# Performance work log

Measured on AMD Instinct MI355X. Metric: run time of the kernel, lower is better.

The kernel has to match this reference:

```python
import jax, jax.numpy as jnp
import numpy as np

LAYERS = (256, 256, 256)
SPLIT = True


def setup_inputs() -> dict:
    key = jax.random.key(0)
    ks = jax.random.split(key, 4)
    B, F0, D = 512, 40, 32
    # field_num with split=True: [40, 128, 128, 128]
    fnum = [F0]
    for i, s in enumerate(LAYERS):
        fnum.append(s // 2 if (SPLIT and i < len(LAYERS) - 1) else (s // 2 if SPLIT else s))
    # conv input channels per layer: fnum[i] * F0
    c1, c2, c3 = fnum[0] * F0, fnum[1] * F0, fnum[2] * F0  # 1600, 5120, 5120
    inputs = jax.random.normal(ks[0], (B, F0, D), dtype=jnp.float32)
    W1 = jax.random.normal(ks[1], (c1, LAYERS[0]), dtype=jnp.float32) / jnp.sqrt(jnp.float32(c1))
    W2 = jax.random.normal(ks[2], (c2, LAYERS[1]), dtype=jnp.float32) / jnp.sqrt(jnp.float32(c2))
    W3 = jax.random.normal(ks[3], (c3, LAYERS[2]), dtype=jnp.float32) / jnp.sqrt(jnp.float32(c3))
    b1 = jnp.zeros((LAYERS[0],), dtype=jnp.float32)
    b2 = jnp.zeros((LAYERS[1],), dtype=jnp.float32)
    b3 = jnp.zeros((LAYERS[2],), dtype=jnp.float32)
    return {"inputs": inputs, "W1": W1, "b1": b1, "W2": W2, "b2": b2, "W3": W3, "b3": b3}


def _cin_forward(inputs, params):
    # inputs: [B, F0, D]
    B, F0, D = inputs.shape
    x0 = inputs
    h = inputs
    outputs = []
    n = len(params)
    for i, (W, b) in enumerate(params):
        # Per-embedding-dim outer product: [B, D, Fi, F0] -> flatten channels.
        z = jnp.einsum('bfd,bgd->bdfg', h, x0).reshape(B, D, -1)
        # 1x1 Conv1D over length-D axis == dense projection on channel axis.
        y = z @ W + b                     # [B, D, size]
        y = jax.nn.relu(y)
        y = jnp.transpose(y, (0, 2, 1))   # [B, size, D]
        if SPLIT and i < n - 1:
            half = y.shape[1] // 2
            outputs.append(y[:, :half, :])
            h = y[:, half:, :]
        else:
            outputs.append(y)
            h = y
    pooled = jnp.concatenate(outputs, axis=1)  # [B, sum_out_fields, D]
    return jnp.sum(pooled, axis=2)             # [B, sum_out_fields]


def reference(inputs, W1, b1, W2, b2, W3, b3):
    return _cin_forward(inputs, [(W1, b1), (W2, b2), (W3, b3)])
```

## Files before the change

### kernel.cpp

```cpp
#include <hip/hip_runtime.h>
#include <hip/hip_bf16.h>


typedef __attribute__((ext_vector_type(8))) short short8;
typedef __attribute__((ext_vector_type(4))) float f32x4;

#define DEVINL __device__ __forceinline__

DEVINL float bf16f(unsigned short u) {
  return __builtin_bit_cast(float, ((unsigned int)u) << 16);
}
DEVINL unsigned short f2bf(float f) {
  unsigned int u = __builtin_bit_cast(unsigned int, f);
  u = u + 0x7FFFu + ((u >> 16) & 1u);
  return (unsigned short)(u >> 16);
}
DEVINL unsigned int pk2(float lo, float hi) {
  union { __hip_bfloat162 h; unsigned int u; } cv;
  cv.h = __float22bfloat162_rn(make_float2(lo, hi));
  return cv.u;
}
DEVINL void gl_lds16(const unsigned short* g, unsigned short* l) {
  __builtin_amdgcn_global_load_lds(
      (const __attribute__((address_space(1))) unsigned int*)g,
      (__attribute__((address_space(3))) unsigned int*)l, 16, 0, 0);
}

__global__ void prep_x(const float* __restrict__ in, unsigned short* __restrict__ xT) {
  __shared__ float lf[40 * 33];
  const int b = blockIdx.x, t = threadIdx.x;
  for (int i = t; i < 1280; i += 256) {
    int g = i >> 5, d = i & 31;
    lf[g * 33 + d] = in[b * 1280 + i];
  }
  __syncthreads();
  for (int i = t; i < 1280; i += 256) {
    int d = i / 40, g = i % 40;
    xT[b * 1280 + i] = f2bf(lf[g * 33 + d]);
  }
}

__global__ void prep_w(const float* __restrict__ W1, const float* __restrict__ W2,
                       const float* __restrict__ W3, unsigned short* __restrict__ Wf1,
                       unsigned short* __restrict__ Wf2, unsigned short* __restrict__ Wf3) {
  __shared__ float lw[8192];
  const int bid = blockIdx.x, t = threadIdx.x;
  const float* W; unsigned short* dst; int s, SPW;
  if (bid < 50)       { W = W1; dst = Wf1; s = bid;       SPW = 10; }
  else if (bid < 210) { W = W2; dst = Wf2; s = bid - 50;  SPW = 32; }
  else                { W = W3; dst = Wf3; s = bid - 210; SPW = 32; }
  const int smod = s % SPW, w = s / SPW;
  for (int i = t; i < 8192; i += 256) {
    int kl = i >> 8, col = i & 255;
    int f = 4 * smod + (kl >> 3);
    int g = 8 * w + (kl & 7);
    lw[i] = W[(f * 40 + g) * 256 + col];
  }
  __syncthreads();
  for (int c = t; c < 1024; c += 256) {
    int grp = c >> 6, ll = c & 63;
    int qq = ll >> 4, col = grp * 16 + (ll & 15);
    unsigned short u[8];
#pragma unroll
    for (int j = 0; j < 8; ++j) u[j] = f2bf(lw[(qq * 8 + j) * 256 + col]);
    uint4 v;
    v.x = (unsigned)u[0] | ((unsigned)u[1] << 16);
    v.y = (unsigned)u[2] | ((unsigned)u[3] << 16);
    v.z = (unsigned)u[4] | ((unsigned)u[5] << 16);
    v.w = (unsigned)u[6] | ((unsigned)u[7] << 16);
    *(uint4*)&dst[s * 8192 + c * 8] = v;
  }
}

template <int LAYER>
__global__ __launch_bounds__(256, 2) void cin_layer(
    const unsigned short* __restrict__ Wfrag, const unsigned short* __restrict__ xT,
    const unsigned short* __restrict__ hIn, const float* __restrict__ bias,
    unsigned short* __restrict__ hOut, float* __restrict__ out) {
  constexpr int FIN = (LAYER == 1) ? 40 : 128;
  constexpr int NKT = FIN * 40 / 32;
  constexpr int SPW = FIN / 4;
  constexpr int HP = 144;

  constexpr int SM_SHORTS = (LAYER == 1) ? (4096 + 5120) : (4096 + 128 * HP);
  __shared__ __align__(16) unsigned short smem[SM_SHORTS];
  unsigned short* Bb = smem;
  unsigned short* hx = smem + 4096;

  const int tid = threadIdx.x;
  const int l = tid & 63;
  const int wid = tid >> 6;
  const int q = l >> 4;
  const int bm = blockIdx.x >> 2;
  const int tn = blockIdx.x & 3;
  const int r0 = bm * 128;
  const int b0 = bm * 4;

  gl_lds16(Wfrag + tn * 2048 + tid * 8, Bb + tid * 8);

  if constexpr (LAYER > 1) {
    const unsigned short* hsrc = hIn + bm * (128 * HP);
#pragma unroll
    for (int i = 0; i < 9; ++i)
      gl_lds16(hsrc + i * 2048 + tid * 8, hx + i * 2048 + tid * 8);
  } else {
    for (int i = tid; i < 640; i += 256)
      *(uint4*)&hx[i * 8] = *(const uint4*)&xT[r0 * 40 + i * 8];
  }

  float xr[2][40];
  if constexpr (LAYER > 1) {
#pragma unroll
    for (int m = 0; m < 2; ++m) {
      const unsigned short* xp = xT + (r0 + wid * 32 + m * 16 + (l & 15)) * 40;
#pragma unroll
      for (int i = 0; i < 5; ++i) {
        uint4 v = *(const uint4*)(xp + i * 8);
        unsigned int uu[4] = {v.x, v.y, v.z, v.w};
#pragma unroll
        for (int d = 0; d < 4; ++d) {
          xr[m][i * 8 + d * 2]     = __builtin_bit_cast(float, uu[d] << 16);
          xr[m][i * 8 + d * 2 + 1] = __builtin_bit_cast(float, uu[d] & 0xffff0000u);
        }
      }
    }
  }

  f32x4 acc[2][4];
#pragma unroll
  for (int m = 0; m < 2; ++m)
#pragma unroll
    for (int n = 0; n < 4; ++n) acc[m][n] = f32x4{0.f, 0.f, 0.f, 0.f};

  asm volatile("s_waitcnt vmcnt(0)" ::: "memory");
  __syncthreads();

#pragma unroll
  for (int w = 0; w < 5; ++w) {
    for (int sm = 0; sm < SPW; ++sm) {
      const int s = w * SPW + sm;
      const int buf = s & 1;
      if (s + 1 < NKT)
        gl_lds16(Wfrag + (s + 1) * 8192 + tn * 2048 + tid * 8,
                 Bb + (buf ^ 1) * 2048 + tid * 8);

      short8 bfr[4];
#pragma unroll
      for (int n = 0; n < 4; ++n)
        bfr[n] = *(const short8*)&Bb[buf * 2048 + n * 512 + l * 8];

#pragma unroll
      for (int m = 0; m < 2; ++m) {
        const int rl = wid * 32 + m * 16 + (l & 15);
        const int f = 4 * sm + q;
        float hf;
        short8 xv;
        if constexpr (LAYER > 1) hf = bf16f(hx[f * HP + rl]);
        else { hf = bf16f(hx[rl * 40 + f]); xv = *(const short8*)&hx[rl * 40 + w * 8]; }
        union { unsigned int u[4]; short8 s8; } A;
#pragma unroll
        for (int jj = 0; jj < 4; ++jj) {
          float p0, p1;
          if constexpr (LAYER > 1) {
            p0 = hf * xr[m][w * 8 + jj * 2];
            p1 = hf * xr[m][w * 8 + jj * 2 + 1];
          } else {
            p0 = hf * bf16f((unsigned short)xv[2 * jj]);
            p1 = hf * bf16f((unsigned short)xv[2 * jj + 1]);
          }
          A.u[jj] = pk2(p0, p1);
        }
#pragma unroll
        for (int n = 0; n < 4; ++n)
          acc[m][n] = __builtin_amdgcn_mfma_f32_16x16x32_bf16(A.s8, bfr[n], acc[m][n], 0, 0, 0);
      }

      asm volatile("s_waitcnt vmcnt(0)" ::: "memory");
      __syncthreads();
    }
  }

  const int colb = tn * 64;
  float bv[4];
#pragma unroll
  for (int n = 0; n < 4; ++n) bv[n] = bias[colb + n * 16 + (l & 15)];

  if (LAYER == 3 || tn < 2) {
    const int jb = (LAYER == 1) ? 0 : (LAYER == 2) ? 128 : 256;
#pragma unroll
    for (int n = 0; n < 4; ++n) {
      const int j = jb + colb + n * 16 + (l & 15);
      float sum = 0.f;
#pragma unroll
      for (int m = 0; m < 2; ++m)
#pragma unroll
        for (int r = 0; r < 4; ++r) sum += fmaxf(acc[m][n][r] + bv[n], 0.f);
      sum += __shfl_xor(sum, 16);
      sum += __shfl_xor(sum, 32);
      if (l < 16) out[(b0 + wid) * 512 + j] = sum;
    }
  } else {
#pragma unroll
    for (int n = 0; n < 4; ++n) {
      const int ff = (tn - 2) * 64 + n * 16 + (l & 15);
#pragma unroll
      for (int m = 0; m < 2; ++m) {
        const int rl = wid * 32 + m * 16 + (l >> 4) * 4;
        float v0 = fmaxf(acc[m][n][0] + bv[n], 0.f);
        float v1 = fmaxf(acc[m][n][1] + bv[n], 0.f);
        float v2 = fmaxf(acc[m][n][2] + bv[n], 0.f);
        float v3 = fmaxf(acc[m][n][3] + bv[n], 0.f);
        uint2 pv;
        pv.x = pk2(v0, v1);
        pv.y = pk2(v2, v3);
        *(uint2*)&hOut[bm * (128 * HP) + ff * HP + rl] = pv;
      }
    }
  }
}

extern "C" void kernel_launch(void* const* d_in, const int* in_sizes, int n_in,
                              void* d_out, int out_size, void* d_ws, size_t ws_size,
                              hipStream_t stream) {
  (void)in_sizes; (void)n_in; (void)out_size; (void)ws_size;
  const float* in = (const float*)d_in[0];
  const float* W1 = (const float*)d_in[1];
  const float* b1 = (const float*)d_in[2];
  const float* W2 = (const float*)d_in[3];
  const float* b2 = (const float*)d_in[4];
  const float* W3 = (const float*)d_in[5];
  const float* b3 = (const float*)d_in[6];
  float* out = (float*)d_out;
  char* ws = (char*)d_ws;

  unsigned short* xT  = (unsigned short*)(ws);
  unsigned short* Wf1 = (unsigned short*)(ws + 1310720);
  unsigned short* Wf2 = (unsigned short*)(ws + 2129920);
  unsigned short* Wf3 = (unsigned short*)(ws + 4751360);
  unsigned short* h1  = (unsigned short*)(ws + 7372800);
  unsigned short* h2  = (unsigned short*)(ws + 12091392);

  prep_x<<<dim3(512), dim3(256), 0, stream>>>(in, xT);
  prep_w<<<dim3(370), dim3(256), 0, stream>>>(W1, W2, W3, Wf1, Wf2, Wf3);
  cin_layer<1><<<dim3(512), dim3(256), 0, stream>>>(Wf1, xT, (const unsigned short*)nullptr, b1, h1, out);
  cin_layer<2><<<dim3(512), dim3(256), 0, stream>>>(Wf2, xT, h1, b2, h2, out);
  cin_layer<3><<<dim3(512), dim3(256), 0, stream>>>(Wf3, xT, h2, b3, (unsigned short*)nullptr, out);
}
```

Measured before the change: 232.3 us.

## Deepen weight prefetch to a 4-stage LDS ring and stage x in LDS

Replaces the double-buffered weight fragments, which waited on vmcnt(0) every k-step, with a 4-slot LDS ring. Weights are prefetched three steps ahead and each step waits only until at most two loads are outstanding. The x tile is now loaded asynchronously into LDS and unpacked per w-chunk, instead of being held as a 2x40 float register array, which lowers register pressure. The cost is more LDS per block and subtle ordering of the vmcnt waits against the h and x loads issued at the start.

```diff
diff --git a/kernel.cpp b/kernel.cpp
--- a/kernel.cpp
+++ b/kernel.cpp
@@ -82,10 +82,11 @@
   constexpr int SPW = FIN / 4;
   constexpr int HP = 144;
 
-  constexpr int SM_SHORTS = (LAYER == 1) ? (4096 + 5120) : (4096 + 128 * HP);
+  constexpr int SM_SHORTS = 8192 + 5120 + ((LAYER > 1) ? 128 * HP : 8);
   __shared__ __align__(16) unsigned short smem[SM_SHORTS];
   unsigned short* Bb = smem;
-  unsigned short* hx = smem + 4096;
+  unsigned short* xs = smem + 8192;
+  unsigned short* hs = smem + 8192 + 5120;
 
   const int tid = threadIdx.x;
   const int l = tid & 63;
@@ -96,89 +97,78 @@
   const int r0 = bm * 128;
   const int b0 = bm * 4;
 
-  gl_lds16(Wfrag + tn * 2048 + tid * 8, Bb + tid * 8);
-
+#pragma unroll
+  for (int s = 0; s < 3; ++s)
+    gl_lds16(Wfrag + s * 8192 + tn * 2048 + tid * 8, Bb + s * 2048 + tid * 8);
+  gl_lds16(xT + r0 * 40 + tid * 8, xs + tid * 8);
+  gl_lds16(xT + r0 * 40 + 2048 + tid * 8, xs + 2048 + tid * 8);
+  if (tid < 128)
+    gl_lds16(xT + r0 * 40 + 4096 + tid * 8, xs + 4096 + tid * 8);
   if constexpr (LAYER > 1) {
     const unsigned short* hsrc = hIn + bm * (128 * HP);
 #pragma unroll
     for (int i = 0; i < 9; ++i)
-      gl_lds16(hsrc + i * 2048 + tid * 8, hx + i * 2048 + tid * 8);
-  } else {
-    for (int i = tid; i < 640; i += 256)
-      *(uint4*)&hx[i * 8] = *(const uint4*)&xT[r0 * 40 + i * 8];
-  }
-
-  float xr[2][40];
-  if constexpr (LAYER > 1) {
+      gl_lds16(hsrc + i * 2048 + tid * 8, hs + i * 2048 + tid * 8);
+  }
+
+  f32x4 acc[2][4];
+#pragma unroll
+  for (int m = 0; m < 2; ++m)
+#pragma unroll
+    for (int n = 0; n < 4; ++n) acc[m][n] = f32x4{0.f, 0.f, 0.f, 0.f};
+
+  const int rl0 = wid * 32 + (l & 15);
+
+  __syncthreads();
+
+#pragma unroll
+  for (int w = 0; w < 5; ++w) {
+    float xw[2][8];
 #pragma unroll
     for (int m = 0; m < 2; ++m) {
-      const unsigned short* xp = xT + (r0 + wid * 32 + m * 16 + (l & 15)) * 40;
-#pragma unroll
-      for (int i = 0; i < 5; ++i) {
-        uint4 v = *(const uint4*)(xp + i * 8);
-        unsigned int uu[4] = {v.x, v.y, v.z, v.w};
-#pragma unroll
-        for (int d = 0; d < 4; ++d) {
-          xr[m][i * 8 + d * 2]     = __builtin_bit_cast(float, uu[d] << 16);
-          xr[m][i * 8 + d * 2 + 1] = __builtin_bit_cast(float, uu[d] & 0xffff0000u);
-        }
+      short8 xv = *(const short8*)&xs[(rl0 + m * 16) * 40 + w * 8];
+#pragma unroll
+      for (int d = 0; d < 4; ++d) {
+        unsigned int uu = ((const unsigned int*)&xv)[d];
+        xw[m][2 * d]     = __builtin_bit_cast(float, uu << 16);
+        xw[m][2 * d + 1] = __builtin_bit_cast(float, uu & 0xffff0000u);
       }
     }
-  }
-
-  f32x4 acc[2][4];
-#pragma unroll
-  for (int m = 0; m < 2; ++m)
-#pragma unroll
-    for (int n = 0; n < 4; ++n) acc[m][n] = f32x4{0.f, 0.f, 0.f, 0.f};
-
-  asm volatile("s_waitcnt vmcnt(0)" ::: "memory");
-  __syncthreads();
-
-#pragma unroll
-  for (int w = 0; w < 5; ++w) {
+
     for (int sm = 0; sm < SPW; ++sm) {
       const int s = w * SPW + sm;
-      const int buf = s & 1;
-      if (s + 1 < NKT)
-        gl_lds16(Wfrag + (s + 1) * 8192 + tn * 2048 + tid * 8,
-                 Bb + (buf ^ 1) * 2048 + tid * 8);
-
+      __builtin_amdgcn_sched_barrier(0);
+      asm volatile("s_waitcnt vmcnt(2)" ::: "memory");
+      __builtin_amdgcn_s_barrier();
+      __builtin_amdgcn_sched_barrier(0);
+
+      const int sn = (s + 3 < NKT) ? (s + 3) : (NKT - 1);
+      gl_lds16(Wfrag + sn * 8192 + tn * 2048 + tid * 8,
+               Bb + ((s + 3) & 3) * 2048 + tid * 8);
+
+      const unsigned short* bb = Bb + (s & 3) * 2048;
       short8 bfr[4];
 #pragma unroll
       for (int n = 0; n < 4; ++n)
-        bfr[n] = *(const short8*)&Bb[buf * 2048 + n * 512 + l * 8];
-
+        bfr[n] = *(const short8*)&bb[n * 512 + l * 8];
+
+      const int f = 4 * sm + q;
 #pragma unroll
       for (int m = 0; m < 2; ++m) {
-        const int rl = wid * 32 + m * 16 + (l & 15);
-        const int f = 4 * sm + q;
-        float hf;
-        short8 xv;
-        if constexpr (LAYER > 1) hf = bf16f(hx[f * HP + rl]);
-        else { hf = bf16f(hx[rl * 40 + f]); xv = *(const short8*)&hx[rl * 40 + w * 8]; }
+        const int rl = rl0 + m * 16;
+        const float hf = (LAYER == 1) ? bf16f(xs[rl * 40 + f])
+                                      : bf16f(hs[f * HP + rl]);
         union { unsigned int u[4]; short8 s8; } A;
 #pragma unroll
-        for (int jj = 0; jj < 4; ++jj) {
-          float p0, p1;
-          if constexpr (LAYER > 1) {
-            p0 = hf * xr[m][w * 8 + jj * 2];
-            p1 = hf * xr[m][w * 8 + jj * 2 + 1];
-          } else {
-            p0 = hf * bf16f((unsigned short)xv[2 * jj]);
-            p1 = hf * bf16f((unsigned short)xv[2 * jj + 1]);
-          }
-          A.u[jj] = pk2(p0, p1);
-        }
+        for (int jj = 0; jj < 4; ++jj)
+          A.u[jj] = pk2(hf * xw[m][2 * jj], hf * xw[m][2 * jj + 1]);
 #pragma unroll
         for (int n = 0; n < 4; ++n)
           acc[m][n] = __builtin_amdgcn_mfma_f32_16x16x32_bf16(A.s8, bfr[n], acc[m][n], 0, 0, 0);
       }
-
-      asm volatile("s_waitcnt vmcnt(0)" ::: "memory");
-      __syncthreads();
-    }
-  }
+    }
+  }
+  asm volatile("s_waitcnt vmcnt(0)" ::: "memory");
 
   const int colb = tn * 64;
   float bv[4];
```

Result: faster. 204.0 us (-12.2%).
